# Kernel optimization log

Measured on AMD Instinct MI355X. Metric: run time of the kernel, lower is better.

The kernel has to match this reference:

```python
import jax, jax.numpy as jnp
import numpy as np

DIM = 768


def setup_inputs() -> dict:
    key = jax.random.key(0)
    k1, k2, k3, k4, k5 = jax.random.split(key, 5)
    lines = jax.random.normal(k1, (32, 512, DIM), dtype=jnp.float32)
    videos = jax.random.normal(k2, (32, 128, DIM), dtype=jnp.float32)
    video_mask = jax.random.randint(k3, (32, 128), 0, 2, dtype=jnp.int32)
    # nn.Linear(dim, dim, bias=False) weights, applied as x @ W.T
    w_q = jax.random.normal(k4, (DIM, DIM), dtype=jnp.float32) * (DIM ** -0.5)
    w_k = jax.random.normal(k5, (DIM, DIM), dtype=jnp.float32) * (DIM ** -0.5)
    return {"lines": lines, "videos": videos, "video_mask": video_mask, "w_q": w_q, "w_k": w_k}


def reference(lines, videos, video_mask, w_q, w_k):
    scale = DIM ** -0.5
    q = jnp.einsum('bld,ed->ble', lines, w_q)   # (B, L, D)
    k = jnp.einsum('bvd,ed->bve', videos, w_k)  # (B, V, D)
    scores = jnp.einsum('bld,bvd->blv', q, k) * scale
    pad = (video_mask == 0)[:, None, :]          # (B, 1, V)
    scores = jnp.where(pad, jnp.float32(-1e9), scores)
    weights = jax.nn.softmax(scores, axis=-1)    # (B, L, V)
    return jnp.einsum('blv,bvd->bld', weights, videos)
```

## Files before the change

### kernel.cpp

```cpp
#include <hip/hip_runtime.h>

#define DIM 768
#define NB  32
#define LQ  512
#define NV  128

typedef unsigned short u16;
typedef unsigned int   u32;
typedef __bf16 bf16x8 __attribute__((ext_vector_type(8)));
typedef float  f32x4  __attribute__((ext_vector_type(4)));
typedef u16    u16x8  __attribute__((ext_vector_type(8)));
typedef u16    u16x4  __attribute__((ext_vector_type(4)));

typedef __attribute__((address_space(1))) const void gvoid;
typedef __attribute__((address_space(3))) void       svoid;

__device__ __forceinline__ u16 f2bf(float f) {
    u32 u = __float_as_uint(f);
    return (u16)((u + 0x7FFFu + ((u >> 16) & 1u)) >> 16);
}

__device__ __forceinline__ bf16x8 ld_frag(const u16* p) {
    return __builtin_bit_cast(bf16x8, *(const u16x8*)p);
}

__device__ __forceinline__ void gld16(const void* g, void* l) {
    __builtin_amdgcn_global_load_lds((gvoid*)g, (svoid*)l, 16, 0, 0);
}

#define W2S    4
#define W2_BLK (36 * W2S)
#define NL_BLK 6144

__global__ __launch_bounds__(256) void prep_kernel(const float* __restrict__ lines,
                                                   const float* __restrict__ w_q,
                                                   const float* __restrict__ w_k,
                                                   const float* __restrict__ videos,
                                                   u16* __restrict__ lbf,
                                                   float* __restrict__ w2f,
                                                   u16* __restrict__ vt2,
                                                   u16* __restrict__ vbf) {
    __shared__ union {
        u16 T[64][136];
        struct { u16 q[128][72]; u16 k[128][72]; } w2s;
    } uL;
    const int bx = blockIdx.x;
    const int t  = threadIdx.x;

    if (bx < W2_BLK) {
        const int tile = bx / W2S, kc = bx % W2S;
        const int m0 = (tile / 6) * 128;
        const int n0 = (tile % 6) * 128;
        const int w    = t >> 6;
        const int lane = t & 63;
        const int quad = lane >> 4;
        const int ln   = lane & 15;
        const int wr   = (w >> 1) * 64;
        const int wc   = (w & 1) * 64;
        f32x4 acc[4][4] = {};
        for (int ks = kc * 3; ks < kc * 3 + 3; ++ks) {
            __syncthreads();
            const int e0 = ks * 64;
#pragma unroll
            for (int p = 0; p < 8; ++p) {
                int f  = t + p * 256;
                int r  = f >> 5;
                int c4 = f & 31;
                float4 xq = *(const float4*)(w_q + (size_t)(e0 + r) * DIM + m0 + c4 * 4);
                float4 xk = *(const float4*)(w_k + (size_t)(e0 + r) * DIM + n0 + c4 * 4);
                int swz = ((r >> 3) ^ ((c4 >> 1) & 7)) * 8 + (r & 7);
                uL.w2s.q[c4 * 4 + 0][swz] = f2bf(xq.x);
                uL.w2s.q[c4 * 4 + 1][swz] = f2bf(xq.y);
                uL.w2s.q[c4 * 4 + 2][swz] = f2bf(xq.z);
                uL.w2s.q[c4 * 4 + 3][swz] = f2bf(xq.w);
                uL.w2s.k[c4 * 4 + 0][swz] = f2bf(xk.x);
                uL.w2s.k[c4 * 4 + 1][swz] = f2bf(xk.y);
                uL.w2s.k[c4 * 4 + 2][swz] = f2bf(xk.z);
                uL.w2s.k[c4 * 4 + 3][swz] = f2bf(xk.w);
            }
            __syncthreads();
#pragma unroll
            for (int kk = 0; kk < 2; ++kk) {
                bf16x8 af[4], bfr[4];
#pragma unroll
                for (int i = 0; i < 4; ++i) {
                    int row = wr + i * 16 + ln;
                    af[i]  = ld_frag(&uL.w2s.q[row][((kk * 4 + quad) ^ ((row >> 3) & 7)) * 8]);
                }
#pragma unroll
                for (int j = 0; j < 4; ++j) {
                    int row = wc + j * 16 + ln;
                    bfr[j] = ld_frag(&uL.w2s.k[row][((kk * 4 + quad) ^ ((row >> 3) & 7)) * 8]);
                }
#pragma unroll
                for (int i = 0; i < 4; ++i)
#pragma unroll
                    for (int j = 0; j < 4; ++j)
                        acc[i][j] = __builtin_amdgcn_mfma_f32_16x16x32_bf16(af[i], bfr[j], acc[i][j], 0, 0, 0);
            }
        }
#pragma unroll
        for (int i = 0; i < 4; ++i)
#pragma unroll
            for (int j = 0; j < 4; ++j)
#pragma unroll
                for (int r = 0; r < 4; ++r)
                    atomicAdd(&w2f[(size_t)(m0 + wr + i * 16 + quad * 4 + r) * DIM +
                                   n0 + wc + j * 16 + ln], acc[i][j][r]);
        return;
    }

    if (bx < W2_BLK + NL_BLK) {
        size_t i = (size_t)(bx - W2_BLK) * 256 + t;
        float4 a = ((const float4*)lines)[i * 2];
        float4 b = ((const float4*)lines)[i * 2 + 1];
        u16x8 o = { f2bf(a.x), f2bf(a.y), f2bf(a.z), f2bf(a.w),
                    f2bf(b.x), f2bf(b.y), f2bf(b.z), f2bf(b.w) };
        ((u16x8*)lbf)[i] = o;
        return;
    }

    const int v  = bx - (W2_BLK + NL_BLK);
    const int b  = v / 12;
    const int d0 = (v % 12) * 64;
    const float* src = videos + (size_t)b * NV * DIM;
#pragma unroll
    for (int p = 0; p < 8; ++p) {
        int f  = t + p * 256;
        int vv = f >> 4;
        int c4 = f & 15;
        float4 x = *(const float4*)(src + (size_t)vv * DIM + d0 + c4 * 4);
        u16x4 o = { f2bf(x.x), f2bf(x.y), f2bf(x.z), f2bf(x.w) };
        uL.T[c4 * 4 + 0][vv] = o[0];
        uL.T[c4 * 4 + 1][vv] = o[1];
        uL.T[c4 * 4 + 2][vv] = o[2];
        uL.T[c4 * 4 + 3][vv] = o[3];
        *(u16x4*)(vbf + ((size_t)b * NV + vv) * DIM + d0 + c4 * 4) = o;
    }
    __syncthreads();
#pragma unroll
    for (int p = 0; p < 4; ++p) {
        int f  = t + p * 256;
        int dl = f >> 4;
        int v8 = f & 15;
        int d  = d0 + dl;
        int it = d >> 7, wv = (d >> 4) & 7, lnn = d & 15;
        int ks = v8 >> 2, qd = v8 & 3;
        int lane = qd * 16 + lnn;
        size_t off = ((((size_t)b * 6 + it) * 8 + wv) * 4 + ks) * 512 + lane * 8;
        *(u16x8*)(vt2 + off) = *(const u16x8*)&uL.T[dl][v8 * 8];
    }
}

__global__ __launch_bounds__(512) void g_kernel(const u16* __restrict__ A,
                                                const float* __restrict__ Wf,
                                                u16* __restrict__ C) {
    __shared__ u16 sA[128][64];
    __shared__ u16 sB[128][72];
    const int t    = threadIdx.x;
    const int w    = t >> 6;
    const int lane = t & 63;
    const int quad = lane >> 4;
    const int ln   = lane & 15;

    int m0, n0;
    {
        int i = blockIdx.x;
        int xcd = i & 7, s = i >> 3;
        m0 = ((s / 6) * 8 + xcd) * 128;
        n0 = (s % 6) * 128;
    }

    const int wr = (w >> 2) * 64;
    const int wc = (w & 3) * 32;
    const int srow   = lane >> 3;
    const int schunk = (lane & 7) ^ srow;

    f32x4 acc[4][2] = {};
#pragma unroll
    for (int ks = 0; ks < 12; ++ks) {
        __syncthreads();
#pragma unroll
        for (int p = 0; p < 2; ++p) {
            int rb = w * 16 + p * 8;
            gld16(A + (size_t)(m0 + rb + srow) * DIM + ks * 64 + schunk * 8, &sA[rb][0]);
        }
#pragma unroll
        for (int p = 0; p < 4; ++p) {
            int idx = t + p * 512;
            int row = idx >> 4, c4 = idx & 15;
            float4 x = *(const float4*)(Wf + (size_t)(n0 + row) * DIM + ks * 64 + c4 * 4);
            u16x4 o = { f2bf(x.x), f2bf(x.y), f2bf(x.z), f2bf(x.w) };
            int swz = ((c4 >> 1) ^ (row & 7)) * 8 + (c4 & 1) * 4;
            *(u16x4*)&sB[row][swz] = o;
        }
        __syncthreads();
#pragma unroll
        for (int kk = 0; kk < 2; ++kk) {
            bf16x8 af[4], bfr[2];
#pragma unroll
            for (int i = 0; i < 4; ++i)
                af[i]  = ld_frag(&sA[wr + i * 16 + ln][((kk * 4 + quad) ^ (ln & 7)) * 8]);
#pragma unroll
            for (int j = 0; j < 2; ++j)
                bfr[j] = ld_frag(&sB[wc + j * 16 + ln][((kk * 4 + quad) ^ (ln & 7)) * 8]);
#pragma unroll
            for (int i = 0; i < 4; ++i)
#pragma unroll
                for (int j = 0; j < 2; ++j)
                    acc[i][j] = __builtin_amdgcn_mfma_f32_16x16x32_bf16(af[i], bfr[j], acc[i][j], 0, 0, 0);
        }
    }
#pragma unroll
    for (int i = 0; i < 4; ++i)
#pragma unroll
        for (int j = 0; j < 2; ++j)
#pragma unroll
            for (int r = 0; r < 4; ++r)
                C[(size_t)(m0 + wr + i * 16 + quad * 4 + r) * DIM + n0 + wc + j * 16 + ln] =
                    f2bf(acc[i][j][r]);
}

__global__ __launch_bounds__(512) void attn_kernel(const u16* __restrict__ Q,
                                                   const u16* __restrict__ K,
                                                   const u16* __restrict__ Vt2,
                                                   const int* __restrict__ mask,
                                                   float* __restrict__ out) {
    int b, l0;
    {
        int i = blockIdx.x;
        int xcd = i & 7, s = i >> 3;
        b  = (s >> 3) * 8 + xcd;
        l0 = (s & 7) * 64;
    }
    const int t    = threadIdx.x;
    const int w    = t >> 6;
    const int lane = t & 63;
    const int quad = lane >> 4;
    const int ln   = lane & 15;

    __shared__ union {
        struct { u16 q[64][64]; u16 k[128][64]; } st;
        float s[64][132];
    } uA;
    __shared__ union {
        struct { u16 q[64][64]; u16 k[128][64]; } st;
        u16 p[64][136];
    } uB;
    __shared__ float sBias[128];

    const u16* Qb = Q + ((size_t)b * LQ + l0) * DIM;
    const u16* Kb = K + (size_t)b * NV * DIM;
    if (t < NV) sBias[t] = mask[b * NV + t] ? 0.0f : -1e9f;

    const int srow   = lane >> 3;
    const int schunk = (lane & 7) ^ srow;

    auto stage = [&](int ks, int sel) {
        u16 (*q)[64] = sel ? uB.st.q : uA.st.q;
        u16 (*k)[64] = sel ? uB.st.k : uA.st.k;
        gld16(Qb + (size_t)(w * 8 + srow) * DIM + ks * 64 + schunk * 8, &q[w * 8][0]);
        gld16(Kb + (size_t)(w * 16 + srow) * DIM + ks * 64 + schunk * 8, &k[w * 16][0]);
        gld16(Kb + (size_t)(w * 16 + 8 + srow) * DIM + ks * 64 + schunk * 8, &k[w * 16 + 8][0]);
    };

    f32x4 accS[4] = {};
    stage(0, 0);
#pragma unroll
    for (int ks = 0; ks < 12; ++ks) {
        __syncthreads();
        if (ks < 11) stage(ks + 1, (ks + 1) & 1);
        u16 (*q)[64] = (ks & 1) ? uB.st.q : uA.st.q;
        u16 (*k)[64] = (ks & 1) ? uB.st.k : uA.st.k;
#pragma unroll
        for (int kk = 0; kk < 2; ++kk) {
            bf16x8 bfr = ld_frag(&k[w * 16 + ln][((kk * 4 + quad) ^ (ln & 7)) * 8]);
#pragma unroll
            for (int i = 0; i < 4; ++i) {
                bf16x8 af = ld_frag(&q[i * 16 + ln][((kk * 4 + quad) ^ (ln & 7)) * 8]);
                accS[i] = __builtin_amdgcn_mfma_f32_16x16x32_bf16(af, bfr, accS[i], 0, 0, 0);
            }
        }
    }
    __syncthreads();
    const float scale = 0.03608439182435161f;
#pragma unroll
    for (int i = 0; i < 4; ++i)
#pragma unroll
        for (int r = 0; r < 4; ++r)
            uA.s[i * 16 + quad * 4 + r][w * 16 + ln] = accS[i][r] * scale;
    __syncthreads();

    {
        const int row = t >> 3, seg = t & 7;
        float vals[16];
        float mx = -3.0e38f;
#pragma unroll
        for (int c = 0; c < 4; ++c) {
            float4 x  = *(const float4*)&uA.s[row][seg * 16 + c * 4];
            float4 bz = *(const float4*)&sBias[seg * 16 + c * 4];
            float a0 = x.x + bz.x, a1 = x.y + bz.y, a2 = x.z + bz.z, a3 = x.w + bz.w;
            vals[c * 4 + 0] = a0; vals[c * 4 + 1] = a1;
            vals[c * 4 + 2] = a2; vals[c * 4 + 3] = a3;
            mx = fmaxf(mx, fmaxf(fmaxf(a0, a1), fmaxf(a2, a3)));
        }
        mx = fmaxf(mx, __shfl_xor(mx, 1));
        mx = fmaxf(mx, __shfl_xor(mx, 2));
        mx = fmaxf(mx, __shfl_xor(mx, 4));
        float sum = 0.0f;
#pragma unroll
        for (int c = 0; c < 16; ++c) { float e = __expf(vals[c] - mx); vals[c] = e; sum += e; }
        sum += __shfl_xor(sum, 1);
        sum += __shfl_xor(sum, 2);
        sum += __shfl_xor(sum, 4);
        const float inv = 1.0f / sum;
        __syncthreads();
#pragma unroll
        for (int h = 0; h < 2; ++h) {
            u16x8 pk;
#pragma unroll
            for (int e = 0; e < 8; ++e) pk[e] = f2bf(vals[h * 8 + e] * inv);
            *(u16x8*)&uB.p[row][seg * 16 + h * 8] = pk;
        }
    }
    __syncthreads();

    bf16x8 paf[4][4];
#pragma unroll
    for (int i = 0; i < 4; ++i)
#pragma unroll
        for (int ks = 0; ks < 4; ++ks)
            paf[i][ks] = ld_frag(&uB.p[i * 16 + ln][ks * 32 + quad * 8]);

    const u16* V2 = Vt2 + (size_t)b * 6 * 8 * 4 * 512;
    float*     Ob = out + ((size_t)b * LQ + l0) * DIM;
    for (int it = 0; it < 6; ++it) {
        f32x4 accO[4] = {};
#pragma unroll
        for (int ks = 0; ks < 4; ++ks) {
            bf16x8 bv = ld_frag(V2 + (((size_t)(it * 8 + w)) * 4 + ks) * 512 + lane * 8);
#pragma unroll
            for (int i = 0; i < 4; ++i)
                accO[i] = __builtin_amdgcn_mfma_f32_16x16x32_bf16(paf[i][ks], bv, accO[i], 0, 0, 0);
        }
#pragma unroll
        for (int i = 0; i < 4; ++i)
#pragma unroll
            for (int r = 0; r < 4; ++r)
                Ob[(size_t)(i * 16 + quad * 4 + r) * DIM + it * 128 + w * 16 + ln] = accO[i][r];
    }
}

extern "C" void kernel_launch(void* const* d_in, const int* in_sizes, int n_in,
                              void* d_out, int out_size, void* d_ws, size_t ws_size,
                              hipStream_t stream) {
    const float* lines  = (const float*)d_in[0];
    const float* videos = (const float*)d_in[1];
    const int*   mask   = (const int*)d_in[2];
    const float* w_q    = (const float*)d_in[3];
    const float* w_k    = (const float*)d_in[4];
    float*       out    = (float*)d_out;

    u16*   gw  = (u16*)d_ws;
    u16*   vt2 = gw  + (size_t)NB * NV * DIM;
    u16*   lbf = vt2 + (size_t)NB * DIM * NV;
    u16*   vbf = lbf + (size_t)NB * LQ * DIM;
    float* w2f = (float*)(vbf + (size_t)NB * NV * DIM);

    hipMemsetAsync(w2f, 0, (size_t)DIM * DIM * sizeof(float), stream);
    prep_kernel<<<W2_BLK + NL_BLK + 384, 256, 0, stream>>>(
        lines, w_q, w_k, videos, lbf, w2f, vt2, vbf);
    g_kernel   <<<192, 512, 0, stream>>>(vbf, w2f, gw);
    attn_kernel<<<256, 512, 0, stream>>>(lbf, gw, vt2, mask, out);
}
```

Before: 163.6 us.

## Fuse lines fp32-to-bf16 conversion into attention kernel and halve query tile

Drops the separate pass in the prep kernel that converted lines to bf16. The attention kernel now loads fp32 lines directly and converts them while staging into swizzled LDS, which removes one full write and read of the bf16 copy. The query tile per block shrinks from 64 to 32 rows, so the grid doubles to 512 blocks for more parallelism. The cost is that each block reloads the K tile for half as many rows, and Q staging becomes synchronous register loads instead of async global-to-LDS copies.

```diff
diff --git a/kernel.cpp b/kernel.cpp
--- a/kernel.cpp
+++ b/kernel.cpp
@@ -30,13 +30,10 @@
 
 #define W2S    4
 #define W2_BLK (36 * W2S)
-#define NL_BLK 6144
-
-__global__ __launch_bounds__(256) void prep_kernel(const float* __restrict__ lines,
-                                                   const float* __restrict__ w_q,
+
+__global__ __launch_bounds__(256) void prep_kernel(const float* __restrict__ w_q,
                                                    const float* __restrict__ w_k,
                                                    const float* __restrict__ videos,
-                                                   u16* __restrict__ lbf,
                                                    float* __restrict__ w2f,
                                                    u16* __restrict__ vt2,
                                                    u16* __restrict__ vbf) {
@@ -110,17 +107,7 @@
         return;
     }
 
-    if (bx < W2_BLK + NL_BLK) {
-        size_t i = (size_t)(bx - W2_BLK) * 256 + t;
-        float4 a = ((const float4*)lines)[i * 2];
-        float4 b = ((const float4*)lines)[i * 2 + 1];
-        u16x8 o = { f2bf(a.x), f2bf(a.y), f2bf(a.z), f2bf(a.w),
-                    f2bf(b.x), f2bf(b.y), f2bf(b.z), f2bf(b.w) };
-        ((u16x8*)lbf)[i] = o;
-        return;
-    }
-
-    const int v  = bx - (W2_BLK + NL_BLK);
+    const int v  = bx - W2_BLK;
     const int b  = v / 12;
     const int d0 = (v % 12) * 64;
     const float* src = videos + (size_t)b * NV * DIM;
@@ -221,7 +208,7 @@
                     f2bf(acc[i][j][r]);
 }
 
-__global__ __launch_bounds__(512) void attn_kernel(const u16* __restrict__ Q,
+__global__ __launch_bounds__(512) void attn_kernel(const float* __restrict__ lines,
                                                    const u16* __restrict__ K,
                                                    const u16* __restrict__ Vt2,
                                                    const int* __restrict__ mask,
@@ -230,8 +217,8 @@
     {
         int i = blockIdx.x;
         int xcd = i & 7, s = i >> 3;
-        b  = (s >> 3) * 8 + xcd;
-        l0 = (s & 7) * 64;
+        b  = (s >> 4) * 8 + xcd;
+        l0 = (s & 15) * 32;
     }
     const int t    = threadIdx.x;
     const int w    = t >> 6;
@@ -240,31 +227,36 @@
     const int ln   = lane & 15;
 
     __shared__ union {
-        struct { u16 q[64][64]; u16 k[128][64]; } st;
-        float s[64][132];
+        struct { u16 q[32][64]; u16 k[128][64]; } st;
+        float s[32][132];
     } uA;
     __shared__ union {
-        struct { u16 q[64][64]; u16 k[128][64]; } st;
-        u16 p[64][136];
+        struct { u16 q[32][64]; u16 k[128][64]; } st;
+        u16 p[32][136];
     } uB;
     __shared__ float sBias[128];
 
-    const u16* Qb = Q + ((size_t)b * LQ + l0) * DIM;
-    const u16* Kb = K + (size_t)b * NV * DIM;
+    const float* Qb = lines + ((size_t)b * LQ + l0) * DIM;
+    const u16*   Kb = K + (size_t)b * NV * DIM;
     if (t < NV) sBias[t] = mask[b * NV + t] ? 0.0f : -1e9f;
 
     const int srow   = lane >> 3;
     const int schunk = (lane & 7) ^ srow;
+    const int qr = w * 4 + (lane >> 4);
+    const int qc = lane & 15;
+    const int qswz = ((qc >> 1) ^ (qr & 7)) * 8 + (qc & 1) * 4;
 
     auto stage = [&](int ks, int sel) {
         u16 (*q)[64] = sel ? uB.st.q : uA.st.q;
         u16 (*k)[64] = sel ? uB.st.k : uA.st.k;
-        gld16(Qb + (size_t)(w * 8 + srow) * DIM + ks * 64 + schunk * 8, &q[w * 8][0]);
+        float4 x = *(const float4*)(Qb + (size_t)qr * DIM + ks * 64 + qc * 4);
+        u16x4 o = { f2bf(x.x), f2bf(x.y), f2bf(x.z), f2bf(x.w) };
+        *(u16x4*)&q[qr][qswz] = o;
         gld16(Kb + (size_t)(w * 16 + srow) * DIM + ks * 64 + schunk * 8, &k[w * 16][0]);
         gld16(Kb + (size_t)(w * 16 + 8 + srow) * DIM + ks * 64 + schunk * 8, &k[w * 16 + 8][0]);
     };
 
-    f32x4 accS[4] = {};
+    f32x4 accS[2] = {};
     stage(0, 0);
 #pragma unroll
     for (int ks = 0; ks < 12; ++ks) {
@@ -276,7 +268,7 @@
         for (int kk = 0; kk < 2; ++kk) {
             bf16x8 bfr = ld_frag(&k[w * 16 + ln][((kk * 4 + quad) ^ (ln & 7)) * 8]);
 #pragma unroll
-            for (int i = 0; i < 4; ++i) {
+            for (int i = 0; i < 2; ++i) {
                 bf16x8 af = ld_frag(&q[i * 16 + ln][((kk * 4 + quad) ^ (ln & 7)) * 8]);
                 accS[i] = __builtin_amdgcn_mfma_f32_16x16x32_bf16(af, bfr, accS[i], 0, 0, 0);
             }
@@ -285,20 +277,20 @@
     __syncthreads();
     const float scale = 0.03608439182435161f;
 #pragma unroll
-    for (int i = 0; i < 4; ++i)
+    for (int i = 0; i < 2; ++i)
 #pragma unroll
         for (int r = 0; r < 4; ++r)
             uA.s[i * 16 + quad * 4 + r][w * 16 + ln] = accS[i][r] * scale;
     __syncthreads();
 
     {
-        const int row = t >> 3, seg = t & 7;
-        float vals[16];
+        const int row = t >> 4, seg = t & 15;
+        float vals[8];
         float mx = -3.0e38f;
 #pragma unroll
-        for (int c = 0; c < 4; ++c) {
-            float4 x  = *(const float4*)&uA.s[row][seg * 16 + c * 4];
-            float4 bz = *(const float4*)&sBias[seg * 16 + c * 4];
+        for (int c = 0; c < 2; ++c) {
+            float4 x  = *(const float4*)&uA.s[row][seg * 8 + c * 4];
+            float4 bz = *(const float4*)&sBias[seg * 8 + c * 4];
             float a0 = x.x + bz.x, a1 = x.y + bz.y, a2 = x.z + bz.z, a3 = x.w + bz.w;
             vals[c * 4 + 0] = a0; vals[c * 4 + 1] = a1;
             vals[c * 4 + 2] = a2; vals[c * 4 + 3] = a3;
@@ -307,27 +299,26 @@
         mx = fmaxf(mx, __shfl_xor(mx, 1));
         mx = fmaxf(mx, __shfl_xor(mx, 2));
         mx = fmaxf(mx, __shfl_xor(mx, 4));
+        mx = fmaxf(mx, __shfl_xor(mx, 8));
         float sum = 0.0f;
 #pragma unroll
-        for (int c = 0; c < 16; ++c) { float e = __expf(vals[c] - mx); vals[c] = e; sum += e; }
+        for (int c = 0; c < 8; ++c) { float e = __expf(vals[c] - mx); vals[c] = e; sum += e; }
         sum += __shfl_xor(sum, 1);
         sum += __shfl_xor(sum, 2);
         sum += __shfl_xor(sum, 4);
+        sum += __shfl_xor(sum, 8);
         const float inv = 1.0f / sum;
         __syncthreads();
-#pragma unroll
-        for (int h = 0; h < 2; ++h) {
-            u16x8 pk;
-#pragma unroll
-            for (int e = 0; e < 8; ++e) pk[e] = f2bf(vals[h * 8 + e] * inv);
-            *(u16x8*)&uB.p[row][seg * 16 + h * 8] = pk;
-        }
+        u16x8 pk;
+#pragma unroll
+        for (int e = 0; e < 8; ++e) pk[e] = f2bf(vals[e] * inv);
+        *(u16x8*)&uB.p[row][seg * 8] = pk;
     }
     __syncthreads();
 
-    bf16x8 paf[4][4];
-#pragma unroll
-    for (int i = 0; i < 4; ++i)
+    bf16x8 paf[2][4];
+#pragma unroll
+    for (int i = 0; i < 2; ++i)
 #pragma unroll
         for (int ks = 0; ks < 4; ++ks)
             paf[i][ks] = ld_frag(&uB.p[i * 16 + ln][ks * 32 + quad * 8]);
@@ -335,16 +326,16 @@
     const u16* V2 = Vt2 + (size_t)b * 6 * 8 * 4 * 512;
     float*     Ob = out + ((size_t)b * LQ + l0) * DIM;
     for (int it = 0; it < 6; ++it) {
-        f32x4 accO[4] = {};
+        f32x4 accO[2] = {};
 #pragma unroll
         for (int ks = 0; ks < 4; ++ks) {
             bf16x8 bv = ld_frag(V2 + (((size_t)(it * 8 + w)) * 4 + ks) * 512 + lane * 8);
 #pragma unroll
-            for (int i = 0; i < 4; ++i)
+            for (int i = 0; i < 2; ++i)
                 accO[i] = __builtin_amdgcn_mfma_f32_16x16x32_bf16(paf[i][ks], bv, accO[i], 0, 0, 0);
         }
 #pragma unroll
-        for (int i = 0; i < 4; ++i)
+        for (int i = 0; i < 2; ++i)
 #pragma unroll
             for (int r = 0; r < 4; ++r)
                 Ob[(size_t)(i * 16 + quad * 4 + r) * DIM + it * 128 + w * 16 + ln] = accO[i][r];
@@ -363,13 +354,11 @@
 
     u16*   gw  = (u16*)d_ws;
     u16*   vt2 = gw  + (size_t)NB * NV * DIM;
-    u16*   lbf = vt2 + (size_t)NB * DIM * NV;
-    u16*   vbf = lbf + (size_t)NB * LQ * DIM;
+    u16*   vbf = vt2 + (size_t)NB * DIM * NV;
     float* w2f = (float*)(vbf + (size_t)NB * NV * DIM);
 
     hipMemsetAsync(w2f, 0, (size_t)DIM * DIM * sizeof(float), stream);
-    prep_kernel<<<W2_BLK + NL_BLK + 384, 256, 0, stream>>>(
-        lines, w_q, w_k, videos, lbf, w2f, vt2, vbf);
+    prep_kernel<<<W2_BLK + 384, 256, 0, stream>>>(w_q, w_k, videos, w2f, vt2, vbf);
     g_kernel   <<<192, 512, 0, stream>>>(vbf, w2f, gw);
-    attn_kernel<<<256, 512, 0, stream>>>(lbf, gw, vt2, mask, out);
-}
+    attn_kernel<<<512, 512, 0, stream>>>(lines, gw, vt2, mask, out);
+}
```

Result: no change. 166.3 us (+1.7%).
